# Kernel tuning notes

Measured on AMD Instinct MI355X. Metric: run time of the kernel, lower is better.

The kernel has to match this reference:

```python
import jax, jax.numpy as jnp
import numpy as np

N_HEADS = 16
THETA = 10000.0


def _rope(x, cos, sin):
    # x: [B,H,S,hd]; pairs are interleaved (x[...,2i], x[...,2i+1]) = complex pair
    xe = x[..., 0::2]
    xo = x[..., 1::2]
    re = xe * cos - xo * sin
    im = xe * sin + xo * cos
    return jnp.stack([re, im], axis=-1).reshape(x.shape)


def setup_inputs() -> dict:
    key = jax.random.key(0)
    k1, k2, k3 = jax.random.split(key, 3)
    B, S, D = 2, 2048, 2048
    x = jax.random.normal(k1, (B, S, D), dtype=jnp.float32)
    Wqkv = jax.random.normal(k2, (D, 3 * D), dtype=jnp.float32) * (D ** -0.5)
    Wo = jax.random.normal(k3, (D, D), dtype=jnp.float32) * (D ** -0.5)
    return {"x": x, "Wqkv": Wqkv, "Wo": Wo}


def reference(x, Wqkv, Wo):
    B, S, D = x.shape
    H = N_HEADS
    hd = D // H
    half = hd // 2

    qkv = x @ Wqkv                                   # [B,S,3D]
    q, k, v = jnp.split(qkv, 3, axis=-1)
    # [B,S,D] -> [B,H,S,hd]
    q = q.reshape(B, S, H, hd).transpose(0, 2, 1, 3)
    k = k.reshape(B, S, H, hd).transpose(0, 2, 1, 3)
    v = v.reshape(B, S, H, hd).transpose(0, 2, 1, 3)

    # RoPE frequencies: thetas = theta^(-2i/hd), freqs = pos outer thetas
    i = jnp.arange(half, dtype=jnp.float32)
    inv = THETA ** (-2.0 * i / hd)
    pos = jnp.arange(S, dtype=jnp.float32)
    freqs = pos[:, None] * inv[None, :]              # [S, half]
    cos = jnp.cos(freqs)[None, None]                 # [1,1,S,half]
    sin = jnp.sin(freqs)[None, None]
    q = _rope(q, cos, sin)
    k = _rope(k, cos, sin)

    scale = 1.0 / jnp.sqrt(jnp.float32(hd))
    scores = jnp.einsum("bhqd,bhkd->bhqk", q, k) * scale
    causal = jnp.tril(jnp.ones((S, S), dtype=bool))
    scores = jnp.where(causal[None, None], scores, -jnp.inf)
    attn = jax.nn.softmax(scores, axis=-1)
    y = jnp.einsum("bhqk,bhkd->bhqd", attn, v)       # [B,H,S,hd]
    y = y.transpose(0, 2, 1, 3).reshape(B, S, D)
    return y @ Wo
```

## Files before the change

kernel.cpp:

```cpp
#include <hip/hip_runtime.h>
#include <hip/hip_bf16.h>

typedef __attribute__((ext_vector_type(4))) float f32x4;
typedef __attribute__((ext_vector_type(8))) short s16x8;
typedef unsigned short u16;
typedef unsigned int u32;

#define MFMA16 __builtin_amdgcn_mfma_f32_16x16x32_bf16

#define GLL16(g, l)                                                        \
  __builtin_amdgcn_global_load_lds(                                        \
      (const __attribute__((address_space(1))) void*)(g),                  \
      (__attribute__((address_space(3))) void*)(l), 16, 0, 0)

__device__ __forceinline__ u16 f2b(float f) {
  u32 x = __builtin_bit_cast(u32, f);
  u32 r = (x + 0x7fffu + ((x >> 16) & 1u)) >> 16;
  return (u16)r;
}
__device__ __forceinline__ float b2f(u16 u) {
  u32 x = ((u32)u) << 16;
  return __builtin_bit_cast(float, x);
}

__global__ __launch_bounds__(256) void k_cvt(const float* __restrict__ in, u16* __restrict__ out) {
  size_t i = ((size_t)blockIdx.x * 256 + threadIdx.x) * 4;
  float4 v = *(const float4*)(in + i);
  ushort4 o; o.x = f2b(v.x); o.y = f2b(v.y); o.z = f2b(v.z); o.w = f2b(v.w);
  *(ushort4*)(out + i) = o;
}

__global__ __launch_bounds__(256) void k_tconv(const float* __restrict__ in, u16* __restrict__ out,
                                               int R, int C) {
  __shared__ u16 tile[64][72];
  int c0 = blockIdx.x * 64, r0 = blockIdx.y * 64;
  int t = threadIdx.x;
#pragma unroll
  for (int p = 0; p < 4; ++p) {
    int idx = p * 1024 + t * 4;
    int row = idx >> 6, col = idx & 63;
    float4 v = *(const float4*)&in[(size_t)(r0 + row) * C + c0 + col];
    tile[row][col]     = f2b(v.x);
    tile[row][col + 1] = f2b(v.y);
    tile[row][col + 2] = f2b(v.z);
    tile[row][col + 3] = f2b(v.w);
  }
  __syncthreads();
#pragma unroll
  for (int p = 0; p < 4; ++p) {
    int idx = p * 1024 + t * 4;
    int row = idx >> 6, col = idx & 63;
    ushort4 o;
    o.x = tile[col][row]; o.y = tile[col + 1][row];
    o.z = tile[col + 2][row]; o.w = tile[col + 3][row];
    *(ushort4*)&out[(size_t)(c0 + row) * R + r0 + col] = o;
  }
}

__global__ __launch_bounds__(256) void k_trv(const u16* __restrict__ v, u16* __restrict__ vt) {
  __shared__ u16 tile[64][72];
  int bh = blockIdx.z;
  int s0 = blockIdx.x * 64, d0 = blockIdx.y * 64;
  const u16* src = v + (size_t)bh * 2048 * 128;
  u16* dst = vt + (size_t)bh * 2048 * 128;
  int t = threadIdx.x;
#pragma unroll
  for (int p = 0; p < 4; ++p) {
    int idx = p * 1024 + t * 4;
    int row = idx >> 6, col = idx & 63;
    ushort4 x = *(const ushort4*)&src[(size_t)(s0 + row) * 128 + d0 + col];
    tile[row][col] = x.x; tile[row][col + 1] = x.y;
    tile[row][col + 2] = x.z; tile[row][col + 3] = x.w;
  }
  __syncthreads();
#pragma unroll
  for (int p = 0; p < 4; ++p) {
    int idx = p * 1024 + t * 4;
    int row = idx >> 6, col = idx & 63;
    ushort4 o;
    o.x = tile[col][row]; o.y = tile[col + 1][row];
    o.z = tile[col + 2][row]; o.w = tile[col + 3][row];
    *(ushort4*)&dst[(size_t)(d0 + row) * 2048 + s0 + col] = o;
  }
}

__global__ __launch_bounds__(256) void k_trig(float2* __restrict__ tab) {
  int t = blockIdx.x * 256 + threadIdx.x;
  int s = t >> 6, i = t & 63;
  float inv = expf(-(float)i * (9.210340371976184f / 64.f));
  float a = (float)s * inv;
  float sn, cs;
  sincosf(a, &sn, &cs);
  tab[t] = make_float2(cs, sn);
}

__global__ __launch_bounds__(256) void k_rope(u16* __restrict__ q, u16* __restrict__ k,
                                              const float2* __restrict__ tab) {
  u16* ptr = blockIdx.y ? k : q;
  size_t tid = (size_t)blockIdx.x * 256 + threadIdx.x;
  int g = (int)(tid & 15);
  int s = (int)((tid >> 4) & 2047);
  int bh = (int)(tid >> 15);
  size_t base = ((size_t)bh * 2048 + s) * 128 + (size_t)g * 8;
  uint4 dv = *(const uint4*)(ptr + base);
  u16* pu = (u16*)&dv;
  const float2* tb = &tab[s * 64 + g * 4];
#pragma unroll
  for (int j = 0; j < 4; ++j) {
    float xe = b2f(pu[2 * j]), xo = b2f(pu[2 * j + 1]);
    float c = tb[j].x, sn = tb[j].y;
    pu[2 * j]     = f2b(xe * c - xo * sn);
    pu[2 * j + 1] = f2b(xe * sn + xo * c);
  }
  *(uint4*)(ptr + base) = dv;
}

__global__ __launch_bounds__(256) void k_gemm_qkv(const u16* __restrict__ A, const u16* __restrict__ Bt,
                                                  u16* __restrict__ qo, u16* __restrict__ ko,
                                                  u16* __restrict__ vo) {
  constexpr int K = 2048;
  __shared__ u16 sa[128][32];
  __shared__ u16 sb[128][32];
  int n0 = blockIdx.x * 128;
  int m0 = blockIdx.y * 128;
  int t = threadIdx.x;
  int lane = t & 63, w = t >> 6;
  int wm = (w >> 1) * 64, wn = (w & 1) * 64;
  int lr = lane & 15, lg = lane >> 4;
  int srow0 = w * 32 + (lane >> 2);
  int srow1 = srow0 + 16;
  int scol = (lane & 3) * 8;
  const u16* gA0 = &A[(size_t)(m0 + srow0) * K + scol];
  const u16* gA1 = &A[(size_t)(m0 + srow1) * K + scol];
  const u16* gB0 = &Bt[(size_t)(n0 + srow0) * K + scol];
  const u16* gB1 = &Bt[(size_t)(n0 + srow1) * K + scol];
  u16* lA0 = &sa[srow0][scol];
  u16* lA1 = &sa[srow1][scol];
  u16* lB0 = &sb[srow0][scol];
  u16* lB1 = &sb[srow1][scol];
  f32x4 acc[4][4] = {};
  for (int k0 = 0; k0 < K; k0 += 32) {
    __syncthreads();
    GLL16(gA0 + k0, lA0); GLL16(gA1 + k0, lA1);
    GLL16(gB0 + k0, lB0); GLL16(gB1 + k0, lB1);
    __syncthreads();
    s16x8 af[4], bf[4];
#pragma unroll
    for (int i = 0; i < 4; ++i) af[i] = *(const s16x8*)&sa[wm + i * 16 + lr][lg * 8];
#pragma unroll
    for (int i = 0; i < 4; ++i) bf[i] = *(const s16x8*)&sb[wn + i * 16 + lr][lg * 8];
#pragma unroll
    for (int mi = 0; mi < 4; ++mi)
#pragma unroll
      for (int ni = 0; ni < 4; ++ni)
        acc[mi][ni] = MFMA16(af[mi], bf[ni], acc[mi][ni], 0, 0, 0);
  }
  int which = blockIdx.x >> 4;
  int h = blockIdx.x & 15;
  u16* dst = which == 0 ? qo : (which == 1 ? ko : vo);
#pragma unroll
  for (int mi = 0; mi < 4; ++mi)
#pragma unroll
    for (int ni = 0; ni < 4; ++ni)
#pragma unroll
      for (int r = 0; r < 4; ++r) {
        int m = m0 + wm + mi * 16 + lg * 4 + r;
        int d = wn + ni * 16 + lr;
        int b = m >> 11, s = m & 2047;
        dst[(((size_t)b * 16 + h) * 2048 + s) * 128 + d] = f2b(acc[mi][ni][r]);
      }
}

__global__ __launch_bounds__(256) void k_gemm_out(const u16* __restrict__ A, const u16* __restrict__ Bt,
                                                  float* __restrict__ C) {
  constexpr int K = 2048, N = 2048;
  __shared__ u16 sa[128][32];
  __shared__ u16 sb[128][32];
  int n0 = blockIdx.x * 128;
  int m0 = blockIdx.y * 128;
  int t = threadIdx.x;
  int lane = t & 63, w = t >> 6;
  int wm = (w >> 1) * 64, wn = (w & 1) * 64;
  int lr = lane & 15, lg = lane >> 4;
  int srow0 = w * 32 + (lane >> 2);
  int srow1 = srow0 + 16;
  int scol = (lane & 3) * 8;
  const u16* gA0 = &A[(size_t)(m0 + srow0) * K + scol];
  const u16* gA1 = &A[(size_t)(m0 + srow1) * K + scol];
  const u16* gB0 = &Bt[(size_t)(n0 + srow0) * K + scol];
  const u16* gB1 = &Bt[(size_t)(n0 + srow1) * K + scol];
  u16* lA0 = &sa[srow0][scol];
  u16* lA1 = &sa[srow1][scol];
  u16* lB0 = &sb[srow0][scol];
  u16* lB1 = &sb[srow1][scol];
  f32x4 acc[4][4] = {};
  for (int k0 = 0; k0 < K; k0 += 32) {
    __syncthreads();
    GLL16(gA0 + k0, lA0); GLL16(gA1 + k0, lA1);
    GLL16(gB0 + k0, lB0); GLL16(gB1 + k0, lB1);
    __syncthreads();
    s16x8 af[4], bf[4];
#pragma unroll
    for (int i = 0; i < 4; ++i) af[i] = *(const s16x8*)&sa[wm + i * 16 + lr][lg * 8];
#pragma unroll
    for (int i = 0; i < 4; ++i) bf[i] = *(const s16x8*)&sb[wn + i * 16 + lr][lg * 8];
#pragma unroll
    for (int mi = 0; mi < 4; ++mi)
#pragma unroll
      for (int ni = 0; ni < 4; ++ni)
        acc[mi][ni] = MFMA16(af[mi], bf[ni], acc[mi][ni], 0, 0, 0);
  }
#pragma unroll
  for (int mi = 0; mi < 4; ++mi)
#pragma unroll
    for (int ni = 0; ni < 4; ++ni)
#pragma unroll
      for (int r = 0; r < 4; ++r) {
        int m = m0 + wm + mi * 16 + lg * 4 + r;
        int n = n0 + wn + ni * 16 + lr;
        C[(size_t)m * N + n] = acc[mi][ni][r];
      }
}

__global__ __launch_bounds__(256) void k_attn(const u16* __restrict__ q, const u16* __restrict__ k,
                                              const u16* __restrict__ vt, u16* __restrict__ y) {
  constexpr int S = 2048, HD = 128;
  __shared__ u16 kt[64][136];
  __shared__ u16 vtl[128][72];
  __shared__ u16 pl[4][16][72];
  int bh = blockIdx.x;
  int qt = (gridDim.y - 1) - blockIdx.y;
  int q0 = qt * 64;
  int t = threadIdx.x, lane = t & 63, w = t >> 6;
  int lr = lane & 15, lg = lane >> 4;
  const size_t base = (size_t)bh * S * HD;

  s16x8 aq[4];
  {
    size_t qrow = base + (size_t)(q0 + w * 16 + lr) * HD;
#pragma unroll
    for (int i = 0; i < 4; ++i) aq[i] = *(const s16x8*)&q[qrow + i * 32 + lg * 8];
  }
  f32x4 o[8] = {};
  float mrow[4] = {-INFINITY, -INFINITY, -INFINITY, -INFINITY};
  float lsum[4] = {};
  const float scale = 0.08838834764831845f;
  int kv_end = q0 + 64;
  for (int kv0 = 0; kv0 < kv_end; kv0 += 64) {
    __syncthreads();
#pragma unroll
    for (int p = 0; p < 4; ++p) {
      int idx = p * 256 + t;
      int row = idx >> 4, c8 = (idx & 15) * 8;
      *(uint4*)&kt[row][c8] = *(const uint4*)&k[base + (size_t)(kv0 + row) * HD + c8];
    }
#pragma unroll
    for (int p = 0; p < 4; ++p) {
      int idx = p * 256 + t;
      int row = idx >> 3, c8 = (idx & 7) * 8;
      *(uint4*)&vtl[row][c8] = *(const uint4*)&vt[base + (size_t)row * S + kv0 + c8];
    }
    __syncthreads();
    f32x4 sf[4] = {};
#pragma unroll
    for (int dstep = 0; dstep < 4; ++dstep)
#pragma unroll
      for (int nt = 0; nt < 4; ++nt) {
        s16x8 bk = *(const s16x8*)&kt[nt * 16 + lr][dstep * 32 + lg * 8];
        sf[nt] = MFMA16(aq[dstep], bk, sf[nt], 0, 0, 0);
      }
    int grow0 = q0 + w * 16 + lg * 4;
    float pmax[4] = {-INFINITY, -INFINITY, -INFINITY, -INFINITY};
#pragma unroll
    for (int nt = 0; nt < 4; ++nt) {
      int col = kv0 + nt * 16 + lr;
#pragma unroll
      for (int r = 0; r < 4; ++r) {
        float sv = sf[nt][r] * scale;
        if (col > grow0 + r) sv = -INFINITY;
        sf[nt][r] = sv;
        pmax[r] = fmaxf(pmax[r], sv);
      }
    }
#pragma unroll
    for (int r = 0; r < 4; ++r) {
#pragma unroll
      for (int off = 1; off < 16; off <<= 1) pmax[r] = fmaxf(pmax[r], __shfl_xor(pmax[r], off));
      float mn = fmaxf(mrow[r], pmax[r]);
      float alpha = __expf(mrow[r] - mn);
      mrow[r] = mn;
      float ps = 0.f;
#pragma unroll
      for (int nt = 0; nt < 4; ++nt) { float e = __expf(sf[nt][r] - mn); sf[nt][r] = e; ps += e; }
#pragma unroll
      for (int off = 1; off < 16; off <<= 1) ps += __shfl_xor(ps, off);
      lsum[r] = lsum[r] * alpha + ps;
#pragma unroll
      for (int dt = 0; dt < 8; ++dt) o[dt][r] *= alpha;
    }
#pragma unroll
    for (int nt = 0; nt < 4; ++nt)
#pragma unroll
      for (int r = 0; r < 4; ++r)
        pl[w][lg * 4 + r][nt * 16 + lr] = f2b(sf[nt][r]);
    asm volatile("s_waitcnt lgkmcnt(0)" ::: "memory");
    __builtin_amdgcn_sched_barrier(0);
    s16x8 pa0 = *(const s16x8*)&pl[w][lr][lg * 8];
    s16x8 pa1 = *(const s16x8*)&pl[w][lr][32 + lg * 8];
#pragma unroll
    for (int dt = 0; dt < 8; ++dt) {
      s16x8 bv0 = *(const s16x8*)&vtl[dt * 16 + lr][lg * 8];
      s16x8 bv1 = *(const s16x8*)&vtl[dt * 16 + lr][32 + lg * 8];
      o[dt] = MFMA16(pa0, bv0, o[dt], 0, 0, 0);
      o[dt] = MFMA16(pa1, bv1, o[dt], 0, 0, 0);
    }
  }
  int b = bh >> 4, h = bh & 15;
#pragma unroll
  for (int dt = 0; dt < 8; ++dt)
#pragma unroll
    for (int r = 0; r < 4; ++r) {
      int srow = q0 + w * 16 + lg * 4 + r;
      float val = o[dt][r] / lsum[r];
      y[((size_t)(b * 2048 + srow)) * 2048 + h * 128 + dt * 16 + lr] = f2b(val);
    }
}

extern "C" void kernel_launch(void* const* d_in, const int* in_sizes, int n_in,
                              void* d_out, int out_size, void* d_ws, size_t ws_size,
                              hipStream_t stream) {
  const float* x    = (const float*)d_in[0];
  const float* wqkv = (const float*)d_in[1];
  const float* wo   = (const float*)d_in[2];
  float* out = (float*)d_out;
  char* ws = (char*)d_ws;
  u16* xb    = (u16*)(ws);
  u16* wqkvt = (u16*)(ws + (size_t)(16)  * 1048576);
  u16* wot   = (u16*)(ws + (size_t)(40)  * 1048576);
  u16* qb    = (u16*)(ws + (size_t)(48)  * 1048576);
  u16* kb    = (u16*)(ws + (size_t)(64)  * 1048576);
  u16* vb    = (u16*)(ws + (size_t)(80)  * 1048576);
  u16* vtb   = (u16*)(ws + (size_t)(96)  * 1048576);
  u16* yb    = (u16*)(ws + (size_t)(112) * 1048576);
  float2* trig = (float2*)(ws + (size_t)(128) * 1048576);

  k_cvt<<<8192, 256, 0, stream>>>(x, xb);
  k_tconv<<<dim3(96, 32), 256, 0, stream>>>(wqkv, wqkvt, 2048, 6144);
  k_tconv<<<dim3(32, 32), 256, 0, stream>>>(wo, wot, 2048, 2048);
  k_trig<<<512, 256, 0, stream>>>(trig);
  k_gemm_qkv<<<dim3(48, 32), 256, 0, stream>>>(xb, wqkvt, qb, kb, vb);
  k_rope<<<dim3(4096, 2), 256, 0, stream>>>(qb, kb, trig);
  k_trv<<<dim3(32, 2, 32), 256, 0, stream>>>(vb, vtb);
  k_attn<<<dim3(32, 32), 256, 0, stream>>>(qb, kb, vtb, yb);
  k_gemm_out<<<dim3(16, 32), 256, 0, stream>>>(yb, wot, out);
}
```

Measured before the change: 347.2 us.

## Prefetch next K/V tile into registers and interleave softmax shuffle reductions

The attention kernel now loads the next K and V^T tile from global memory into registers while the current tile is being computed, then writes those registers to LDS at the start of the next iteration. This hides global load latency behind the QK^T and PV MFMAs. The per-row shuffle reductions are restructured so the four rows reduce together, which exposes more independent work per step. s_setprio brackets around the MFMA loops raise wave priority during matrix work. Holding 8 uint4 prefetch registers raises register pressure, which may lower occupancy.

```diff
diff --git a/kernel.cpp b/kernel.cpp
--- a/kernel.cpp
+++ b/kernel.cpp
@@ -234,6 +234,8 @@
   int t = threadIdx.x, lane = t & 63, w = t >> 6;
   int lr = lane & 15, lg = lane >> 4;
   const size_t base = (size_t)bh * S * HD;
+  const u16* kbh = k + base;
+  const u16* vbh = vt + base;
 
   s16x8 aq[4];
   {
@@ -246,22 +248,34 @@
   float lsum[4] = {};
   const float scale = 0.08838834764831845f;
   int kv_end = q0 + 64;
+
+  uint4 pk[4], pv[4];
+#pragma unroll
+  for (int p = 0; p < 4; ++p) {
+    int idx = p * 256 + t;
+    pk[p] = *(const uint4*)&kbh[(size_t)(idx >> 4) * HD + (idx & 15) * 8];
+    pv[p] = *(const uint4*)&vbh[(size_t)(idx >> 3) * S + (idx & 7) * 8];
+  }
   for (int kv0 = 0; kv0 < kv_end; kv0 += 64) {
     __syncthreads();
 #pragma unroll
     for (int p = 0; p < 4; ++p) {
       int idx = p * 256 + t;
-      int row = idx >> 4, c8 = (idx & 15) * 8;
-      *(uint4*)&kt[row][c8] = *(const uint4*)&k[base + (size_t)(kv0 + row) * HD + c8];
-    }
-#pragma unroll
-    for (int p = 0; p < 4; ++p) {
-      int idx = p * 256 + t;
-      int row = idx >> 3, c8 = (idx & 7) * 8;
-      *(uint4*)&vtl[row][c8] = *(const uint4*)&vt[base + (size_t)row * S + kv0 + c8];
-    }
-    __syncthreads();
+      *(uint4*)&kt[idx >> 4][(idx & 15) * 8] = pk[p];
+      *(uint4*)&vtl[idx >> 3][(idx & 7) * 8] = pv[p];
+    }
+    __syncthreads();
+    if (kv0 + 64 < kv_end) {
+      int kn = kv0 + 64;
+#pragma unroll
+      for (int p = 0; p < 4; ++p) {
+        int idx = p * 256 + t;
+        pk[p] = *(const uint4*)&kbh[(size_t)(kn + (idx >> 4)) * HD + (idx & 15) * 8];
+        pv[p] = *(const uint4*)&vbh[(size_t)(idx >> 3) * S + kn + (idx & 7) * 8];
+      }
+    }
     f32x4 sf[4] = {};
+    __builtin_amdgcn_s_setprio(1);
 #pragma unroll
     for (int dstep = 0; dstep < 4; ++dstep)
 #pragma unroll
@@ -269,6 +283,7 @@
         s16x8 bk = *(const s16x8*)&kt[nt * 16 + lr][dstep * 32 + lg * 8];
         sf[nt] = MFMA16(aq[dstep], bk, sf[nt], 0, 0, 0);
       }
+    __builtin_amdgcn_s_setprio(0);
     int grow0 = q0 + w * 16 + lg * 4;
     float pmax[4] = {-INFINITY, -INFINITY, -INFINITY, -INFINITY};
 #pragma unroll
@@ -283,20 +298,28 @@
       }
     }
 #pragma unroll
+    for (int off = 1; off < 16; off <<= 1)
+#pragma unroll
+      for (int r = 0; r < 4; ++r) pmax[r] = fmaxf(pmax[r], __shfl_xor(pmax[r], off));
+    float alpha[4], ps[4];
+#pragma unroll
     for (int r = 0; r < 4; ++r) {
-#pragma unroll
-      for (int off = 1; off < 16; off <<= 1) pmax[r] = fmaxf(pmax[r], __shfl_xor(pmax[r], off));
       float mn = fmaxf(mrow[r], pmax[r]);
-      float alpha = __expf(mrow[r] - mn);
+      alpha[r] = __expf(mrow[r] - mn);
       mrow[r] = mn;
-      float ps = 0.f;
-#pragma unroll
-      for (int nt = 0; nt < 4; ++nt) { float e = __expf(sf[nt][r] - mn); sf[nt][r] = e; ps += e; }
-#pragma unroll
-      for (int off = 1; off < 16; off <<= 1) ps += __shfl_xor(ps, off);
-      lsum[r] = lsum[r] * alpha + ps;
-#pragma unroll
-      for (int dt = 0; dt < 8; ++dt) o[dt][r] *= alpha;
+      ps[r] = 0.f;
+#pragma unroll
+      for (int nt = 0; nt < 4; ++nt) { float e = __expf(sf[nt][r] - mn); sf[nt][r] = e; ps[r] += e; }
+    }
+#pragma unroll
+    for (int off = 1; off < 16; off <<= 1)
+#pragma unroll
+      for (int r = 0; r < 4; ++r) ps[r] += __shfl_xor(ps[r], off);
+#pragma unroll
+    for (int r = 0; r < 4; ++r) {
+      lsum[r] = lsum[r] * alpha[r] + ps[r];
+#pragma unroll
+      for (int dt = 0; dt < 8; ++dt) o[dt][r] *= alpha[r];
     }
 #pragma unroll
     for (int nt = 0; nt < 4; ++nt)
@@ -307,6 +330,7 @@
     __builtin_amdgcn_sched_barrier(0);
     s16x8 pa0 = *(const s16x8*)&pl[w][lr][lg * 8];
     s16x8 pa1 = *(const s16x8*)&pl[w][lr][32 + lg * 8];
+    __builtin_amdgcn_s_setprio(1);
 #pragma unroll
     for (int dt = 0; dt < 8; ++dt) {
       s16x8 bv0 = *(const s16x8*)&vtl[dt * 16 + lr][lg * 8];
@@ -314,6 +338,7 @@
       o[dt] = MFMA16(pa0, bv0, o[dt], 0, 0, 0);
       o[dt] = MFMA16(pa1, bv1, o[dt], 0, 0, 0);
     }
+    __builtin_amdgcn_s_setprio(0);
   }
   int b = bh >> 4, h = bh & 15;
 #pragma unroll
```

Measured after the change: 399.5 us. 1.15x slower.
